# Kernel tuning notes

Measured on AMD Instinct MI355X. Metric: run time of the kernel, lower is better.

Reference implementation:

```python
import jax, jax.numpy as jnp
import numpy as np

ROPE_BASE = 10000.0


def _rope(x):
    # x: (B, S, H, D) -- rotate-half RoPE applied per head over the sequence dim
    B, S, H, D = x.shape
    half = D // 2
    inv_freq = 1.0 / (ROPE_BASE ** (jnp.arange(half, dtype=jnp.float32) / half))
    ang = jnp.arange(S, dtype=jnp.float32)[:, None] * inv_freq[None, :]  # (S, half)
    cos = jnp.cos(ang)[None, :, None, :].astype(x.dtype)
    sin = jnp.sin(ang)[None, :, None, :].astype(x.dtype)
    x1, x2 = x[..., :half], x[..., half:]
    return jnp.concatenate([x1 * cos - x2 * sin, x2 * cos + x1 * sin], axis=-1)


def setup_inputs() -> dict:
    key = jax.random.key(0)
    ks = jax.random.split(key, 7)
    B, S, D = 8, 1024, 512
    HD = 512  # num_heads * key_dim = 8 * 64
    scale = 0.02
    return {
        "query": jax.random.normal(ks[0], (B, S, D), dtype=jnp.float32),
        "value": jax.random.normal(ks[1], (B, S, D), dtype=jnp.float32),
        "key_in": jax.random.normal(ks[2], (B, S, D), dtype=jnp.float32),
        "Wq": jax.random.normal(ks[3], (D, HD), dtype=jnp.float32) * scale,
        "Wk": jax.random.normal(ks[4], (D, HD), dtype=jnp.float32) * scale,
        "Wv": jax.random.normal(ks[5], (D, HD), dtype=jnp.float32) * scale,
        "Wo": jax.random.normal(ks[6], (HD, D), dtype=jnp.float32) * scale,
    }


def reference(query, value, key_in, Wq, Wk, Wv, Wo):
    H, Dh = 8, 64
    B, Sq, _ = query.shape
    Sk = key_in.shape[1]
    # QKV projections, split heads: (B, S, H, Dh)
    q = (query @ Wq).reshape(B, Sq, H, Dh)
    v = (value @ Wv).reshape(B, Sk, H, Dh)
    k = (key_in @ Wk).reshape(B, Sk, H, Dh)
    # inline RoPE on q and k (applied before head transpose, as in the original)
    q = _rope(q)
    k = _rope(k)
    # scaled dot-product attention with causal mask
    q = q * (1.0 / jnp.sqrt(jnp.asarray(Dh, q.dtype)))
    scores = jnp.einsum("bqhd,bkhd->bhqk", q, k)  # (B, H, Sq, Sk)
    causal = jnp.tril(jnp.ones((Sq, Sk), dtype=bool))[None, None]
    scores = jnp.where(causal, scores, jnp.asarray(-1e9, scores.dtype))
    probs = jax.nn.softmax(scores, axis=-1)
    out = jnp.einsum("bhqk,bkhd->bqhd", probs, v)  # (B, Sq, H, Dh)
    out = out.reshape(B, Sq, H * Dh) @ Wo  # output projection
    return out
```

## Files before the change

kernel.cpp:

```cpp
#include <hip/hip_runtime.h>
#include <hip/hip_bf16.h>
#include <stdint.h>

#define DEV static __device__ __forceinline__

typedef __attribute__((ext_vector_type(8)))  short    s16x8;
typedef __attribute__((ext_vector_type(4)))  short    s16x4;
typedef __attribute__((ext_vector_type(8)))  __bf16   bf16x8;
typedef __attribute__((ext_vector_type(4)))  float    f32x4;
typedef __attribute__((ext_vector_type(16))) float    f32x16;
typedef __attribute__((ext_vector_type(2)))  unsigned u32x2;
typedef __attribute__((ext_vector_type(4)))  unsigned u32x4;

DEV short f2b(float f){
  union{float f; uint32_t i;} x; x.f = f;
  uint32_t r = x.i + 0x7FFFu + ((x.i >> 16) & 1u);
  return (short)(r >> 16);
}
DEV bf16x8 as_bf(s16x8 v){ return __builtin_bit_cast(bf16x8, v); }
DEV float fexp2(float x){ return __builtin_amdgcn_exp2f(x); }
DEV f32x4 mf(s16x8 a, s16x8 b, f32x4 c){
  return __builtin_amdgcn_mfma_f32_16x16x32_bf16(as_bf(a), as_bf(b), c, 0, 0, 0);
}
DEV f32x16 mf32(s16x8 a, s16x8 b, f32x16 c){
  return __builtin_amdgcn_mfma_f32_32x32x16_bf16(as_bf(a), as_bf(b), c, 0, 0, 0);
}

DEV void gload_lds16(const void* g, void* l){
  __builtin_amdgcn_global_load_lds((const __attribute__((address_space(1))) void*)g,
                                   (__attribute__((address_space(3))) void*)l, 16, 0, 0);
}

#if __has_builtin(__builtin_amdgcn_permlane32_swap)
DEV void pswap2(unsigned a, unsigned b, unsigned& x, unsigned& y){
  u32x2 rr = __builtin_amdgcn_permlane32_swap(a, b, false, false);
  x = rr[0]; y = rr[1];
}
DEV float partner32(float v, int hi){
  unsigned u = __builtin_bit_cast(unsigned, v);
  u32x2 rr = __builtin_amdgcn_permlane32_swap(u, u, false, false);
  return __builtin_bit_cast(float, hi ? rr[0] : rr[1]);
}
#else
DEV void pswap2(unsigned a, unsigned b, unsigned& x, unsigned& y){
  unsigned pa_ = (unsigned)__shfl_xor((int)a, 32, 64);
  unsigned pb_ = (unsigned)__shfl_xor((int)b, 32, 64);
  int lo = ((threadIdx.x & 63) < 32);
  x = lo ? a   : pb_;
  y = lo ? pa_ : b;
}
DEV float partner32(float v, int hi){ (void)hi; return __shfl_xor(v, 32, 64); }
#endif

__global__ __launch_bounds__(256) void k_wt4(const float* __restrict__ w0,
                                             const float* __restrict__ w1,
                                             const float* __restrict__ w2,
                                             const float* __restrict__ w3,
                                             short* __restrict__ wt){
  __shared__ float tile[32][33];
  int z = blockIdx.z;
  const float* w = (z == 0) ? w0 : (z == 1) ? w1 : (z == 2) ? w2 : w3;
  short* o = wt + (size_t)z * 262144;
  int bx = blockIdx.x * 32, by = blockIdx.y * 32;
  int tx = threadIdx.x, ty = threadIdx.y;
  for (int j = 0; j < 32; j += 8)
    tile[ty + j][tx] = w[(size_t)(by + ty + j) * 512 + bx + tx];
  __syncthreads();
  for (int j = 0; j < 32; j += 8)
    o[(size_t)(bx + ty + j) * 512 + by + tx] = f2b(tile[tx][ty + j]);
}

__global__ __launch_bounds__(256) void k_table(float* __restrict__ tab){
  int idx = blockIdx.x * 256 + threadIdx.x;
  int s = idx >> 5, j = idx & 31;
  float inv = __expf(-(float)j * (1.0f / 32.0f) * logf(10000.0f));
  float ang = (float)s * inv;
  tab[idx * 2 + 0] = cosf(ang);
  tab[idx * 2 + 1] = sinf(ang);
}

__global__ __launch_bounds__(256) void k_qkv(const float* __restrict__ Xq,
                                             const float* __restrict__ Xk,
                                             const float* __restrict__ Xv,
                                             const short* __restrict__ Wcat,
                                             const float* __restrict__ tab,
                                             short* __restrict__ Qa,
                                             short* __restrict__ Ka,
                                             short* __restrict__ Vt){
  __shared__ __align__(16) short Al[2][128 * 32];
  __shared__ __align__(16) short Bl[2][128 * 32];
  const int t = threadIdx.x;
  const int w = t >> 6, lane = t & 63, fr = lane & 15, fg = lane >> 4;
  const int sel = blockIdx.y >> 2;
  const float* X = (sel == 0) ? Xq : (sel == 1) ? Xk : Xv;
  const int bm = blockIdx.x * 128, bn = blockIdx.y * 128;
  const int wm = (w >> 1) * 64, wn = (w & 1) * 64;
  const int r8 = t >> 2, c8 = (t & 3) * 8;

  float4 ua[4];
  auto ldA = [&](int k0){
    const float* s0 = X + (size_t)(bm + (t >> 2)) * 512 + k0 + c8;
    const float* s1 = s0 + 64 * 512;
    ua[0] = *(const float4*)(s0);
    ua[1] = *(const float4*)(s0 + 4);
    ua[2] = *(const float4*)(s1);
    ua[3] = *(const float4*)(s1 + 4);
  };
  auto wrA = [&](int buf){
    s16x8 p0 = { f2b(ua[0].x), f2b(ua[0].y), f2b(ua[0].z), f2b(ua[0].w),
                 f2b(ua[1].x), f2b(ua[1].y), f2b(ua[1].z), f2b(ua[1].w) };
    s16x8 p1 = { f2b(ua[2].x), f2b(ua[2].y), f2b(ua[2].z), f2b(ua[2].w),
                 f2b(ua[3].x), f2b(ua[3].y), f2b(ua[3].z), f2b(ua[3].w) };
    *(s16x8*)(&Al[buf][(t >> 2) * 32 + c8])        = p0;
    *(s16x8*)(&Al[buf][(64 + (t >> 2)) * 32 + c8]) = p1;
  };
  auto stB = [&](int buf, int k0){
#pragma unroll
    for (int j = 0; j < 2; j++)
      gload_lds16(Wcat + (size_t)(bn + j * 64 + r8) * 512 + k0 + c8,
                  &Bl[buf][j * 2048 + w * 512]);
  };

  f32x4 acc[4][4] = {};
  ldA(0); stB(0, 0); wrA(0);
  __syncthreads();
  int cur = 0;
  for (int t16 = 0; t16 < 16; ++t16){
    const int k0n = (t16 + 1) * 32;
    if (t16 < 15){ ldA(k0n); stB(cur ^ 1, k0n); }
    s16x8 af[4], bv[4];
#pragma unroll
    for (int f = 0; f < 4; f++){
      af[f] = *(const s16x8*)(&Al[cur][(wm + f * 16 + fr) * 32 + fg * 8]);
      bv[f] = *(const s16x8*)(&Bl[cur][(wn + f * 16 + fr) * 32 + fg * 8]);
    }
#pragma unroll
    for (int i = 0; i < 4; i++)
#pragma unroll
      for (int jj = 0; jj < 4; jj++)
        acc[i][jj] = mf(af[i], bv[jj], acc[i][jj]);
    if (t16 < 15) wrA(cur ^ 1);
    __syncthreads();
    cur ^= 1;
  }

  const int row0 = bm + wm + fg * 4;
  const int b = row0 >> 10;
  const int s_base = row0 & 1023;
  const int hh = (((blockIdx.y & 3) * 128) + wn) >> 6;
  if (sel < 2){
    const float scale = (sel == 0) ? 0.125f * 1.44269504f : 1.0f;
    short* out = (sel == 0) ? Qa : Ka;
#pragma unroll
    for (int i = 0; i < 4; i++)
#pragma unroll
      for (int jj = 0; jj < 2; jj++){
        int d = jj * 16 + fr;
#pragma unroll
        for (int r = 0; r < 4; r++){
          int s = s_base + i * 16 + r;
          float2 cs = *(const float2*)(tab + (size_t)(s * 32 + d) * 2);
          float x1 = acc[i][jj][r], x2 = acc[i][jj + 2][r];
          size_t ob = ((size_t)((b * 8 + hh) * 1024 + s)) * 64 + d;
          out[ob]      = f2b((x1 * cs.x - x2 * cs.y) * scale);
          out[ob + 32] = f2b((x2 * cs.x + x1 * cs.y) * scale);
        }
      }
  } else {
#pragma unroll
    for (int i = 0; i < 4; i++)
#pragma unroll
      for (int jj = 0; jj < 4; jj++){
        int d = jj * 16 + fr;
        s16x4 pk;
#pragma unroll
        for (int r = 0; r < 4; r++) pk[r] = f2b(acc[i][jj][r]);
        size_t ob = ((size_t)((b * 8 + hh) * 64 + d)) * 1024 + s_base + i * 16;
        *(s16x4*)(Vt + ob) = pk;
      }
  }
}

__global__ __launch_bounds__(128) void k_attn(const short* __restrict__ Qb,
                                              const short* __restrict__ Kb,
                                              const short* __restrict__ Vt,
                                              short* __restrict__ O){
  __shared__ __align__(16) short KL[2][4096];
  __shared__ __align__(16) short VL[2][4096];
  const int bid = blockIdx.x;
  const int podr[16] = {15,14,13,12, 0,1,2,3, 11,10,9,8, 4,5,6,7};
  const int Bi = podr[bid >> 6];
  const int bh = bid & 63;
  const int B0 = Bi * 64;
  const int t = threadIdx.x, w = t >> 6, lane = t & 63;
  const int col = lane & 31, hi = lane >> 5;
  const short* Qp = Qb + (size_t)bh * 65536;
  const short* Kp = Kb + (size_t)bh * 65536;
  const short* Vp = Vt + (size_t)bh * 65536;
  const int qrow = B0 + 2 * col + w;

  s16x8 qb[4];
#pragma unroll
  for (int ks = 0; ks < 4; ks++)
    qb[ks] = *(const s16x8*)(Qp + (size_t)qrow * 64 + ks * 16 + hi * 8);

  int crow[16];
#pragma unroll
  for (int r = 0; r < 16; r++) crow[r] = (r & 3) + 8 * (r >> 2) + 4 * hi;

  f32x16 oacc[2] = {};
  float m = -1e30f, l = 0.f;

  auto stage = [&](int buf, int kv0){
#pragma unroll
    for (int R = 0; R < 4; R++){
      int lin = R * 128 + w * 64 + lane;
      int row = lin >> 3, slot = lin & 7;
      int gs = ((slot ^ (row & 7)) * 8);
      gload_lds16(Kp + (size_t)(kv0 + row) * 64 + gs, &KL[buf][(R * 128 + w * 64) * 8]);
      gload_lds16(Vp + (size_t)row * 1024 + kv0 + gs, &VL[buf][(R * 128 + w * 64) * 8]);
    }
  };

  stage(0, 0);
  __syncthreads();

  int cur = 0;
  for (int kv0 = 0; kv0 <= B0; kv0 += 64){
    if (kv0 < B0) stage(cur ^ 1, kv0 + 64);
    f32x16 sc[2];
#pragma unroll
    for (int f = 0; f < 2; f++){
      f32x16 s = {};
      int row = f * 32 + col, rx = row & 7;
#pragma unroll
      for (int ks = 0; ks < 4; ks++){
        s16x8 ka = *(const s16x8*)(&KL[cur][row * 64 + ((ks * 2 + hi) ^ rx) * 8]);
        s = mf32(ka, qb[ks], s);
      }
      sc[f] = s;
    }
    if (kv0 == B0){
#pragma unroll
      for (int f = 0; f < 2; f++)
#pragma unroll
        for (int r = 0; r < 16; r++){
          int kv = kv0 + f * 32 + crow[r];
          if (kv > qrow) sc[f][r] = -1e30f;
        }
    }
    float tm = -1e30f;
#pragma unroll
    for (int f = 0; f < 2; f++)
#pragma unroll
      for (int r = 0; r < 16; r++) tm = fmaxf(tm, sc[f][r]);
    tm = fmaxf(tm, partner32(tm, hi));
    if (!__all(tm <= m + 8.f)){
      float mn = fmaxf(m, tm);
      float corr = fexp2(m - mn);
      m = mn;
      l *= corr;
      float cpv[16];
#pragma unroll
      for (int r = 0; r < 16; r++) cpv[r] = __shfl(corr, crow[r], 64);
#pragma unroll
      for (int r = 0; r < 16; r++){ oacc[0][r] *= cpv[r]; oacc[1][r] *= cpv[r]; }
    }
    float rs = 0.f;
    unsigned wq[2][8];
#pragma unroll
    for (int f = 0; f < 2; f++)
#pragma unroll
      for (int i = 0; i < 8; i++){
        float p0 = fexp2(sc[f][2 * i]     - m);
        float p1 = fexp2(sc[f][2 * i + 1] - m);
        rs += p0 + p1;
        wq[f][i] = (unsigned)(uint16_t)f2b(p0) | ((unsigned)(uint16_t)f2b(p1) << 16);
      }
    rs += partner32(rs, hi);
    l += rs;
    s16x8 pa[4];
#pragma unroll
    for (int f = 0; f < 2; f++)
#pragma unroll
      for (int half = 0; half < 2; half++){
        unsigned w0, w1, w2, w3;
        pswap2(wq[f][half * 4 + 0], wq[f][half * 4 + 2], w0, w2);
        pswap2(wq[f][half * 4 + 1], wq[f][half * 4 + 3], w1, w3);
        u32x4 uv = { w0, w1, w2, w3 };
        pa[f * 2 + half] = __builtin_bit_cast(s16x8, uv);
      }
#pragma unroll
    for (int ks = 0; ks < 4; ks++)
#pragma unroll
      for (int df = 0; df < 2; df++){
        int row = df * 32 + col;
        s16x8 vb = *(const s16x8*)(&VL[cur][row * 64 + ((ks * 2 + hi) ^ (row & 7)) * 8]);
        oacc[df] = mf32(pa[ks], vb, oacc[df]);
      }
    if (kv0 < B0) __syncthreads();
    cur ^= 1;
  }

  const int b = bh >> 3, h = bh & 7;
  float lf[16];
#pragma unroll
  for (int r = 0; r < 16; r++) lf[r] = __shfl(l, crow[r], 64);
#pragma unroll
  for (int r = 0; r < 16; r++){
    int qq = B0 + 2 * crow[r] + w;
    float inv = 1.0f / lf[r];
    O[(size_t)(b * 1024 + qq) * 512 + h * 64 + col]      = f2b(oacc[0][r] * inv);
    O[(size_t)(b * 1024 + qq) * 512 + h * 64 + 32 + col] = f2b(oacc[1][r] * inv);
  }
}

__global__ __launch_bounds__(256) void k_gemm_out(const short* __restrict__ X,
                                                  const short* __restrict__ Wt,
                                                  float* __restrict__ C){
  __shared__ __align__(16) short Al[2][128 * 32];
  __shared__ __align__(16) short Bl[2][128 * 32];
  const int t = threadIdx.x;
  const int w = t >> 6, lane = t & 63, fr = lane & 15, fg = lane >> 4;
  const int bm = blockIdx.x * 128, bn = blockIdx.y * 128;
  const int wm = (w >> 1) * 64, wn = (w & 1) * 64;
  const int r8 = t >> 2, c8 = (t & 3) * 8;

  auto stage = [&](int buf, int k0){
#pragma unroll
    for (int j = 0; j < 2; j++){
      gload_lds16(X  + (size_t)(bm + j * 64 + r8) * 512 + k0 + c8, &Al[buf][j * 2048 + w * 512]);
      gload_lds16(Wt + (size_t)(bn + j * 64 + r8) * 512 + k0 + c8, &Bl[buf][j * 2048 + w * 512]);
    }
  };

  f32x4 acc[4][4] = {};
  stage(0, 0);
  __syncthreads();
  int cur = 0;
  for (int t16 = 0; t16 < 16; ++t16){
    if (t16 < 15) stage(cur ^ 1, (t16 + 1) * 32);
    s16x8 af[4], bv[4];
#pragma unroll
    for (int f = 0; f < 4; f++){
      af[f] = *(const s16x8*)(&Al[cur][(wm + f * 16 + fr) * 32 + fg * 8]);
      bv[f] = *(const s16x8*)(&Bl[cur][(wn + f * 16 + fr) * 32 + fg * 8]);
    }
#pragma unroll
    for (int i = 0; i < 4; i++)
#pragma unroll
      for (int jj = 0; jj < 4; jj++)
        acc[i][jj] = mf(af[i], bv[jj], acc[i][jj]);
    __syncthreads();
    cur ^= 1;
  }
  const int row0 = bm + wm + fg * 4;
  const int col0 = bn + wn + fr;
#pragma unroll
  for (int i = 0; i < 4; i++)
#pragma unroll
    for (int jj = 0; jj < 4; jj++)
#pragma unroll
      for (int r = 0; r < 4; r++)
        C[(size_t)(row0 + i * 16 + r) * 512 + col0 + jj * 16] = acc[i][jj][r];
}

extern "C" void kernel_launch(void* const* d_in, const int* in_sizes, int n_in,
                              void* d_out, int out_size, void* d_ws, size_t ws_size,
                              hipStream_t stream){
  const float* query  = (const float*)d_in[0];
  const float* value  = (const float*)d_in[1];
  const float* key_in = (const float*)d_in[2];
  const float* Wq     = (const float*)d_in[3];
  const float* Wk     = (const float*)d_in[4];
  const float* Wv     = (const float*)d_in[5];
  const float* Wo     = (const float*)d_in[6];

  char* ws = (char*)d_ws;
  const size_t MB = 1ull << 20;
  short* Oa   = (short*)(ws);
  short* Wcat = (short*)(ws + 24 * MB);
  float* tab  = (float*)(ws + 26 * MB);
  short* Qa   = (short*)(ws + 26 * MB + 256 * 1024);
  short* Ka   = (short*)((char*)Qa + 8 * MB);
  short* Va   = (short*)((char*)Ka + 8 * MB);
  short* Wot  = Wcat + 786432;

  k_wt4<<<dim3(16, 16, 4), dim3(32, 8), 0, stream>>>(Wq, Wk, Wv, Wo, Wcat);
  k_table<<<128, 256, 0, stream>>>(tab);

  k_qkv<<<dim3(64, 12), 256, 0, stream>>>(query, key_in, value, Wcat, tab, Qa, Ka, Va);

  k_attn<<<1024, 128, 0, stream>>>(Qa, Ka, Va, Oa);

  k_gemm_out<<<dim3(64, 4), 256, 0, stream>>>(Oa, Wot, (float*)d_out);
}
```

Baseline: 78.78 us.

## Retile QKV GEMM to full-width N per block and swizzle LDS layouts

The QKV projection now launches 384 blocks of 512 threads. Each block computes 64 rows against all 512 output columns of one projection, with one wave per head, so each A tile is converted from fp32 to bf16 only once instead of four times. Both QKV and the output GEMM use XOR-swizzled LDS layouts to avoid bank conflicts, and the output GEMM doubles its K step to 64 per stage, halving the barrier count. The cost is larger LDS use per block and higher register pressure under the new launch bounds, which could lower occupancy.

```diff
diff --git a/kernel.cpp b/kernel.cpp
--- a/kernel.cpp
+++ b/kernel.cpp
@@ -79,46 +79,41 @@
   tab[idx * 2 + 1] = sinf(ang);
 }
 
-__global__ __launch_bounds__(256) void k_qkv(const float* __restrict__ Xq,
-                                             const float* __restrict__ Xk,
-                                             const float* __restrict__ Xv,
-                                             const short* __restrict__ Wcat,
-                                             const float* __restrict__ tab,
-                                             short* __restrict__ Qa,
-                                             short* __restrict__ Ka,
-                                             short* __restrict__ Vt){
-  __shared__ __align__(16) short Al[2][128 * 32];
-  __shared__ __align__(16) short Bl[2][128 * 32];
-  const int t = threadIdx.x;
-  const int w = t >> 6, lane = t & 63, fr = lane & 15, fg = lane >> 4;
-  const int sel = blockIdx.y >> 2;
+__global__ __launch_bounds__(512, 4) void k_qkv(const float* __restrict__ Xq,
+                                                const float* __restrict__ Xk,
+                                                const float* __restrict__ Xv,
+                                                const short* __restrict__ Wcat,
+                                                const float* __restrict__ tab,
+                                                short* __restrict__ Qa,
+                                                short* __restrict__ Ka,
+                                                short* __restrict__ Vt){
+  __shared__ __align__(16) short Af[2][2048];
+  __shared__ __align__(16) short Bf[2][16384];
+  const int t = threadIdx.x, w = t >> 6, lane = t & 63, fr = lane & 15, fg = lane >> 4;
+  const int bid = blockIdx.x;
+  const int sel = bid >> 7;
+  const int m0 = (bid & 127) * 64;
   const float* X = (sel == 0) ? Xq : (sel == 1) ? Xk : Xv;
-  const int bm = blockIdx.x * 128, bn = blockIdx.y * 128;
-  const int wm = (w >> 1) * 64, wn = (w & 1) * 64;
-  const int r8 = t >> 2, c8 = (t & 3) * 8;
-
-  float4 ua[4];
-  auto ldA = [&](int k0){
-    const float* s0 = X + (size_t)(bm + (t >> 2)) * 512 + k0 + c8;
-    const float* s1 = s0 + 64 * 512;
-    ua[0] = *(const float4*)(s0);
-    ua[1] = *(const float4*)(s0 + 4);
-    ua[2] = *(const float4*)(s1);
-    ua[3] = *(const float4*)(s1 + 4);
-  };
+  const short* Wp = Wcat + (size_t)sel * 262144;
+
+  const int ar = t >> 3;
+  const int ak = (t & 7) * 4;
+  const int aoff = (ar >> 1) * 64 + ((((ar & 1) * 4 + ((t & 7) >> 1)) ^ ((ar >> 1) & 7))) * 8
+                   + (t & 1) * 4;
+  float4 ua;
+  auto ldA = [&](int k0){ ua = *(const float4*)(X + (size_t)(m0 + ar) * 512 + k0 + ak); };
   auto wrA = [&](int buf){
-    s16x8 p0 = { f2b(ua[0].x), f2b(ua[0].y), f2b(ua[0].z), f2b(ua[0].w),
-                 f2b(ua[1].x), f2b(ua[1].y), f2b(ua[1].z), f2b(ua[1].w) };
-    s16x8 p1 = { f2b(ua[2].x), f2b(ua[2].y), f2b(ua[2].z), f2b(ua[2].w),
-                 f2b(ua[3].x), f2b(ua[3].y), f2b(ua[3].z), f2b(ua[3].w) };
-    *(s16x8*)(&Al[buf][(t >> 2) * 32 + c8])        = p0;
-    *(s16x8*)(&Al[buf][(64 + (t >> 2)) * 32 + c8]) = p1;
+    s16x4 pk = { f2b(ua.x), f2b(ua.y), f2b(ua.z), f2b(ua.w) };
+    *(s16x4*)(&Af[buf][aoff]) = pk;
   };
   auto stB = [&](int buf, int k0){
 #pragma unroll
-    for (int j = 0; j < 2; j++)
-      gload_lds16(Wcat + (size_t)(bn + j * 64 + r8) * 512 + k0 + c8,
-                  &Bl[buf][j * 2048 + w * 512]);
+    for (int q = 0; q < 4; q++){
+      int lin = q * 512 + t;
+      int pair = lin >> 3, s8 = lin & 7, u = s8 ^ (pair & 7);
+      int col = pair * 2 + (u >> 2), kq = (u & 3) * 8;
+      gload_lds16(Wp + (size_t)col * 512 + k0 + kq, &Bf[buf][(q * 512 + w * 64) * 8]);
+    }
   };
 
   f32x4 acc[4][4] = {};
@@ -131,8 +126,12 @@
     s16x8 af[4], bv[4];
 #pragma unroll
     for (int f = 0; f < 4; f++){
-      af[f] = *(const s16x8*)(&Al[cur][(wm + f * 16 + fr) * 32 + fg * 8]);
-      bv[f] = *(const s16x8*)(&Bl[cur][(wn + f * 16 + fr) * 32 + fg * 8]);
+      int row = f * 16 + fr;
+      int s8 = (((row & 1) * 4 + fg) ^ ((row >> 1) & 7));
+      af[f] = *(const s16x8*)(&Af[cur][(row >> 1) * 64 + s8 * 8]);
+      int ca = w * 64 + f * 16 + fr;
+      int s8b = (((ca & 1) * 4 + fg) ^ ((ca >> 1) & 7));
+      bv[f] = *(const s16x8*)(&Bf[cur][(ca >> 1) * 64 + s8b * 8]);
     }
 #pragma unroll
     for (int i = 0; i < 4; i++)
@@ -144,10 +143,9 @@
     cur ^= 1;
   }
 
-  const int row0 = bm + wm + fg * 4;
+  const int row0 = m0 + fg * 4;
   const int b = row0 >> 10;
   const int s_base = row0 & 1023;
-  const int hh = (((blockIdx.y & 3) * 128) + wn) >> 6;
   if (sel < 2){
     const float scale = (sel == 0) ? 0.125f * 1.44269504f : 1.0f;
     short* out = (sel == 0) ? Qa : Ka;
@@ -161,7 +159,7 @@
           int s = s_base + i * 16 + r;
           float2 cs = *(const float2*)(tab + (size_t)(s * 32 + d) * 2);
           float x1 = acc[i][jj][r], x2 = acc[i][jj + 2][r];
-          size_t ob = ((size_t)((b * 8 + hh) * 1024 + s)) * 64 + d;
+          size_t ob = ((size_t)((b * 8 + w) * 1024 + s)) * 64 + d;
           out[ob]      = f2b((x1 * cs.x - x2 * cs.y) * scale);
           out[ob + 32] = f2b((x2 * cs.x + x1 * cs.y) * scale);
         }
@@ -175,7 +173,7 @@
         s16x4 pk;
 #pragma unroll
         for (int r = 0; r < 4; r++) pk[r] = f2b(acc[i][jj][r]);
-        size_t ob = ((size_t)((b * 8 + hh) * 64 + d)) * 1024 + s_base + i * 16;
+        size_t ob = ((size_t)((b * 8 + w) * 64 + d)) * 1024 + s_base + i * 16;
         *(s16x4*)(Vt + ob) = pk;
       }
   }
@@ -315,22 +313,24 @@
   }
 }
 
-__global__ __launch_bounds__(256) void k_gemm_out(const short* __restrict__ X,
-                                                  const short* __restrict__ Wt,
-                                                  float* __restrict__ C){
-  __shared__ __align__(16) short Al[2][128 * 32];
-  __shared__ __align__(16) short Bl[2][128 * 32];
+__global__ __launch_bounds__(256, 2) void k_gemm_out(const short* __restrict__ X,
+                                                     const short* __restrict__ Wt,
+                                                     float* __restrict__ C){
+  __shared__ __align__(16) short Al[2][8192];
+  __shared__ __align__(16) short Bl[2][8192];
   const int t = threadIdx.x;
   const int w = t >> 6, lane = t & 63, fr = lane & 15, fg = lane >> 4;
   const int bm = blockIdx.x * 128, bn = blockIdx.y * 128;
   const int wm = (w >> 1) * 64, wn = (w & 1) * 64;
-  const int r8 = t >> 2, c8 = (t & 3) * 8;
 
   auto stage = [&](int buf, int k0){
 #pragma unroll
-    for (int j = 0; j < 2; j++){
-      gload_lds16(X  + (size_t)(bm + j * 64 + r8) * 512 + k0 + c8, &Al[buf][j * 2048 + w * 512]);
-      gload_lds16(Wt + (size_t)(bn + j * 64 + r8) * 512 + k0 + c8, &Bl[buf][j * 2048 + w * 512]);
+    for (int q = 0; q < 4; q++){
+      int lin = q * 256 + t;
+      int row = lin >> 3, sl = lin & 7;
+      int gs = (sl ^ (row & 7)) * 8;
+      gload_lds16(X  + (size_t)(bm + row) * 512 + k0 + gs, &Al[buf][(q * 256 + w * 64) * 8]);
+      gload_lds16(Wt + (size_t)(bn + row) * 512 + k0 + gs, &Bl[buf][(q * 256 + w * 64) * 8]);
     }
   };
 
@@ -338,19 +338,24 @@
   stage(0, 0);
   __syncthreads();
   int cur = 0;
-  for (int t16 = 0; t16 < 16; ++t16){
-    if (t16 < 15) stage(cur ^ 1, (t16 + 1) * 32);
-    s16x8 af[4], bv[4];
-#pragma unroll
-    for (int f = 0; f < 4; f++){
-      af[f] = *(const s16x8*)(&Al[cur][(wm + f * 16 + fr) * 32 + fg * 8]);
-      bv[f] = *(const s16x8*)(&Bl[cur][(wn + f * 16 + fr) * 32 + fg * 8]);
-    }
-#pragma unroll
-    for (int i = 0; i < 4; i++)
-#pragma unroll
-      for (int jj = 0; jj < 4; jj++)
-        acc[i][jj] = mf(af[i], bv[jj], acc[i][jj]);
+  for (int t8 = 0; t8 < 8; ++t8){
+    if (t8 < 7) stage(cur ^ 1, (t8 + 1) * 64);
+#pragma unroll
+    for (int kk = 0; kk < 2; kk++){
+      s16x8 af[4], bv[4];
+#pragma unroll
+      for (int f = 0; f < 4; f++){
+        int rowa = wm + f * 16 + fr;
+        af[f] = *(const s16x8*)(&Al[cur][rowa * 64 + ((kk * 4 + fg) ^ (rowa & 7)) * 8]);
+        int rowb = wn + f * 16 + fr;
+        bv[f] = *(const s16x8*)(&Bl[cur][rowb * 64 + ((kk * 4 + fg) ^ (rowb & 7)) * 8]);
+      }
+#pragma unroll
+      for (int i = 0; i < 4; i++)
+#pragma unroll
+        for (int jj = 0; jj < 4; jj++)
+          acc[i][jj] = mf(af[i], bv[jj], acc[i][jj]);
+    }
     __syncthreads();
     cur ^= 1;
   }
@@ -389,7 +394,7 @@
   k_wt4<<<dim3(16, 16, 4), dim3(32, 8), 0, stream>>>(Wq, Wk, Wv, Wo, Wcat);
   k_table<<<128, 256, 0, stream>>>(tab);
 
-  k_qkv<<<dim3(64, 12), 256, 0, stream>>>(query, key_in, value, Wcat, tab, Qa, Ka, Va);
+  k_qkv<<<384, 512, 0, stream>>>(query, key_in, value, Wcat, tab, Qa, Ka, Va);
 
   k_attn<<<1024, 128, 0, stream>>>(Qa, Ka, Va, Oa);
 
```

After: 81.20 us. 3.1% more time.
